# Optimization experiments

Hardware: AMD Instinct MI355X
Metric: run time of the kernel (lower is better)

Reference implementation:

```python
import jax, jax.numpy as jnp
import numpy as np

SIZE = 512
ATTN = 64      # per-head attention_size
OUT = 64       # per-head output_size
HEADS = 8

def setup_inputs() -> dict:
    key = jax.random.key(0)
    ks = jax.random.split(key, 7)
    s = 0.02
    return {
        "x":  jax.random.normal(ks[0], (4, 2048, SIZE), dtype=jnp.float32),
        "Wq": jax.random.normal(ks[1], (SIZE, ATTN * HEADS), dtype=jnp.float32) * s,
        "bq": jax.random.normal(ks[2], (ATTN * HEADS,), dtype=jnp.float32) * s,
        "Wk": jax.random.normal(ks[3], (SIZE, ATTN), dtype=jnp.float32) * s,  # shared key, no bias
        "Wv": jax.random.normal(ks[4], (SIZE, OUT * HEADS), dtype=jnp.float32) * s,
        "bv": jax.random.normal(ks[5], (OUT * HEADS,), dtype=jnp.float32) * s,
    }

def reference(x, Wq, bq, Wk, Wv, bv):
    B, S, _ = x.shape
    q = (x @ Wq + bq).reshape(B, S, HEADS, ATTN)   # (B,S,H,A)
    k = x @ Wk                                      # (B,S,A) shared across heads
    v = (x @ Wv + bv).reshape(B, S, HEADS, OUT)     # (B,S,H,O)
    # NOTE: original divides by sqrt(seq_len), not sqrt(head_dim)
    scale = 1.0 / np.sqrt(S).astype(np.float32)
    scores = jnp.einsum("bqha,bka->bhqk", q, k) * scale  # (B,H,S,S)
    causal = jnp.tril(jnp.ones((S, S), dtype=bool))
    scores = jnp.where(causal, scores, -jnp.inf)
    attn = jax.nn.softmax(scores, axis=-1)
    out = jnp.einsum("bhqk,bkho->bqho", attn, v)    # (B,S,H,O)
    return out.reshape(B, S, HEADS * OUT)
```

## Files before the change

kernel.cpp:

```cpp
#include <hip/hip_runtime.h>
#include <math.h>


typedef _Float16 half8 __attribute__((ext_vector_type(8)));
typedef _Float16 half4 __attribute__((ext_vector_type(4)));
typedef float float4v __attribute__((ext_vector_type(4)));
typedef unsigned int u32;

#define SCL2E 0.031885926f

__device__ inline float4v mfma16(half8 a, half8 b, float4v c) {
    return __builtin_amdgcn_mfma_f32_16x16x32_f16(a, b, c, 0, 0, 0);
}
__device__ inline void load16(const _Float16* g, _Float16* l) {
    __builtin_amdgcn_global_load_lds((const __attribute__((address_space(1))) u32*)g,
                                     (__attribute__((address_space(3))) u32*)l, 16, 0, 0);
}

__global__ __launch_bounds__(256) void prep(
    const float* __restrict__ x, const float* __restrict__ Wq,
    const float* __restrict__ Wk, const float* __restrict__ Wv,
    _Float16* __restrict__ xh, _Float16* __restrict__ wqt,
    _Float16* __restrict__ wkt, _Float16* __restrict__ wvt) {
    const int bid = blockIdx.x;
    if (bid < 2048) {
        size_t base = (size_t)bid * 2048 + (size_t)threadIdx.x * 8;
        const float4* xp = (const float4*)(x + base);
        float4 f0 = xp[0], f1 = xp[1];
        half8 h = {(_Float16)f0.x, (_Float16)f0.y, (_Float16)f0.z, (_Float16)f0.w,
                   (_Float16)f1.x, (_Float16)f1.y, (_Float16)f1.z, (_Float16)f1.w};
        *(half8*)(xh + base) = h;
    } else {
        int r = bid - 2048;
        const float* W; _Float16* WT; int N, bx, by;
        if (r < 256)      { W = Wq; WT = wqt; N = 512; bx = r & 15; by = r >> 4; }
        else if (r < 288) { r -= 256; W = Wk; WT = wkt; N = 64;  bx = r & 1;  by = r >> 1; }
        else              { r -= 288; W = Wv; WT = wvt; N = 512; bx = r & 15; by = r >> 4; }
        __shared__ float T[32][33];
        const int tx = threadIdx.x & 31, ty = threadIdx.x >> 5;
        const int n0 = bx * 32, k0 = by * 32;
#pragma unroll
        for (int i = 0; i < 4; ++i)
            T[ty + 8 * i][tx] = W[(size_t)(k0 + ty + 8 * i) * N + n0 + tx];
        __syncthreads();
#pragma unroll
        for (int i = 0; i < 4; ++i)
            WT[(size_t)(n0 + ty + 8 * i) * 512 + k0 + tx] = (_Float16)T[tx][ty + 8 * i];
    }
}

__global__ __launch_bounds__(256) void qkv_gemm(
    const _Float16* __restrict__ xh,
    const _Float16* __restrict__ wqt, const _Float16* __restrict__ wkt,
    const _Float16* __restrict__ wvt,
    const float* __restrict__ bq, const float* __restrict__ bv,
    _Float16* __restrict__ q_ws, _Float16* __restrict__ kt_ws, _Float16* __restrict__ vt_ws) {
    __shared__ __align__(16) _Float16 Xs[2][8192];
    __shared__ __align__(16) _Float16 Ws[2][4096];

    const int m0 = blockIdx.x * 128;
    const int nt = blockIdx.y;
    const _Float16* WT;
    const float* bias;
    if (nt < 8)       { WT = wqt + (size_t)nt * 64 * 512; bias = bq + nt * 64; }
    else if (nt == 8) { WT = wkt;                          bias = nullptr; }
    else              { WT = wvt + (size_t)(nt - 9) * 64 * 512; bias = bv + (nt - 9) * 64; }

    const int tid = threadIdx.x;
    const int w = tid >> 6, lane = tid & 63, quad = lane >> 4, cl = lane & 15;
    const int lrow = lane >> 3;
    const int lgc = (lane & 7) ^ lrow;
    const _Float16* xg = xh + (size_t)(m0 + lrow) * 512 + lgc * 8;
    const _Float16* wg = WT + (size_t)lrow * 512 + lgc * 8;

    const int g0 = (quad ^ (cl & 7)) << 3;
    const int g1 = ((quad ^ 4) ^ (cl & 7)) << 3;

    float4v acc[2][4] = {};

#pragma unroll
    for (int c = 0; c < 4; ++c) {
        int cc = w * 4 + c;
        load16(xg + (size_t)cc * 8 * 512, Xs[0] + cc * 512);
    }
#pragma unroll
    for (int c = 0; c < 2; ++c) {
        int cc = w * 2 + c;
        load16(wg + (size_t)cc * 8 * 512, Ws[0] + cc * 512);
    }

    for (int ki = 0; ki < 8; ++ki) {
        const int cb = ki & 1, nb = cb ^ 1;
        __syncthreads();
        if (ki < 7) {
            const int kk = (ki + 1) * 64;
#pragma unroll
            for (int c = 0; c < 4; ++c) {
                int cc = w * 4 + c;
                load16(xg + (size_t)cc * 8 * 512 + kk, Xs[nb] + cc * 512);
            }
#pragma unroll
            for (int c = 0; c < 2; ++c) {
                int cc = w * 2 + c;
                load16(wg + (size_t)cc * 8 * 512 + kk, Ws[nb] + cc * 512);
            }
        }
#pragma unroll
        for (int c = 0; c < 2; ++c) {
            const int g = c ? g1 : g0;
#pragma unroll
            for (int s = 0; s < 2; ++s) {
                half8 a = *(const half8*)(Xs[cb] + (w * 32 + s * 16 + cl) * 64 + g);
#pragma unroll
                for (int j = 0; j < 4; ++j) {
                    half8 b = *(const half8*)(Ws[cb] + (j * 16 + cl) * 64 + g);
                    acc[s][j] = mfma16(a, b, acc[s][j]);
                }
            }
        }
    }

    if (nt < 8) {
#pragma unroll
        for (int s = 0; s < 2; ++s)
#pragma unroll
            for (int j = 0; j < 4; ++j)
#pragma unroll
                for (int r = 0; r < 4; ++r) {
                    int lr = w * 32 + s * 16 + quad * 4 + r;
                    int col = j * 16 + cl;
                    q_ws[(size_t)(m0 + lr) * 512 + nt * 64 + col] =
                        (_Float16)((acc[s][j][r] + bias[col]) * SCL2E);
                }
    } else if (nt == 8) {
#pragma unroll
        for (int s = 0; s < 2; ++s)
#pragma unroll
            for (int j = 0; j < 4; ++j)
#pragma unroll
                for (int r = 0; r < 4; ++r) {
                    int grow = m0 + w * 32 + s * 16 + quad * 4 + r;
                    int b = grow >> 11, t = (grow >> 6) & 31, row = grow & 63;
                    int col = j * 16 + cl;
                    kt_ws[((size_t)(b * 32 + t) << 12) + row * 64 +
                          (((col >> 3) ^ (row & 7)) << 3) + (col & 7)] = (_Float16)acc[s][j][r];
                }
    } else {
        const int h = nt - 9;
#pragma unroll
        for (int s = 0; s < 2; ++s)
#pragma unroll
            for (int j = 0; j < 4; ++j)
#pragma unroll
                for (int r = 0; r < 4; ++r) {
                    int grow = m0 + w * 32 + s * 16 + quad * 4 + r;
                    int b = grow >> 11, t = (grow >> 6) & 31, row = grow & 63;
                    int o = j * 16 + cl;
                    int kap = ((row & 15) << 2) + (row >> 4);
                    vt_ws[(((size_t)(b * 8 + h) * 32 + t) << 12) + o * 64 +
                          (((kap >> 3) ^ (o & 7)) << 3) + (kap & 7)] =
                        (_Float16)(acc[s][j][r] + bias[o]);
                }
    }
}

__global__ __launch_bounds__(512, 2) void attn(
    const _Float16* __restrict__ q_ws, const _Float16* __restrict__ kt_ws,
    const _Float16* __restrict__ vt_ws, float* __restrict__ out) {
    __shared__ __align__(16) _Float16 Ks[2][2][4096];
    __shared__ __align__(16) _Float16 VTs[2][2][4096];
    __shared__ __align__(16) _Float16 Ps[8][1024];

    const int bh = blockIdx.x, b = bh >> 3, h = bh & 7;
    const int p = 31 - blockIdx.y;
    const int q0 = p * 64;
    const int nmax = (p + 2) >> 1;

    const int bS = b * 2048;
    const int tid = threadIdx.x;
    const int w = tid >> 6, lane = tid & 63, quad = lane >> 4, cl = lane & 15;
    const int g = w >> 2, wl = w & 3;
    const int tbase = g ? nmax : 0;
    const int nit = g ? (p + 1 - nmax) : nmax;

    const _Float16* kbase = kt_ws + ((size_t)(b * 32) << 12);
    const _Float16* vbase = vt_ws + ((size_t)((b * 8 + h) * 32) << 12);

    const int g0 = (quad ^ (cl & 7)) << 3;
    const int g1 = ((quad ^ 4) ^ (cl & 7)) << 3;
    const int so0 = wl * 1024 + lane * 8;

    const _Float16* qbase = q_ws + (size_t)(bS + q0 + wl * 16 + cl) * 512 + h * 64;
    half8 qa0 = *(const half8*)(qbase + quad * 8);
    half8 qa1 = *(const half8*)(qbase + 32 + quad * 8);

    float4v oacc[4] = {};
    float l_run[4] = {0.f, 0.f, 0.f, 0.f};

    _Float16* KsG = &Ks[g][0][0];
    _Float16* VsG = &VTs[g][0][0];

    auto stageK = [&](int tile, int buf) {
        const _Float16* kt = kbase + ((size_t)tile << 12);
        load16(kt + so0,       KsG + buf * 4096 + wl * 1024);
        load16(kt + so0 + 512, KsG + buf * 4096 + wl * 1024 + 512);
    };
    auto stageV = [&](int tile, int buf) {
        const _Float16* vt = vbase + ((size_t)tile << 12);
        load16(vt + so0,       VsG + buf * 4096 + wl * 1024);
        load16(vt + so0 + 512, VsG + buf * 4096 + wl * 1024 + 512);
    };
    auto qk_sm = [&](int tg, int buf) {
        const _Float16* KB = KsG + buf * 4096;
        if (tg != p) {
            float4v sfr[4];
#pragma unroll
            for (int j = 0; j < 4; ++j) {
                const _Float16* kr = KB + (j * 16 + cl) * 64;
                half8 b0 = *(const half8*)(kr + g0);
                half8 b1 = *(const half8*)(kr + g1);
                float4v a_ = {0.f, 0.f, 0.f, 0.f};
                a_ = mfma16(qa0, b0, a_);
                a_ = mfma16(qa1, b1, a_);
                sfr[j] = a_;
            }
#pragma unroll
            for (int r = 0; r < 4; ++r) {
                float p0 = exp2f(sfr[0][r]), p1 = exp2f(sfr[1][r]);
                float p2 = exp2f(sfr[2][r]), p3 = exp2f(sfr[3][r]);
                l_run[r] += (p0 + p1) + (p2 + p3);
                int rr = quad * 4 + r;
                half4 ph = {(_Float16)p0, (_Float16)p1, (_Float16)p2, (_Float16)p3};
                *(half4*)&Ps[w][rr * 64 + ((((cl >> 1) ^ (rr & 7)) << 3) | ((cl & 1) << 2))] = ph;
            }
        } else {
            const int jmax = wl;
            float4v sfr[4];
#pragma unroll
            for (int j = 0; j < 4; ++j) {
                if (j <= jmax) {
                    const _Float16* kr = KB + (j * 16 + cl) * 64;
                    half8 b0 = *(const half8*)(kr + g0);
                    half8 b1 = *(const half8*)(kr + g1);
                    float4v a_ = {0.f, 0.f, 0.f, 0.f};
                    a_ = mfma16(qa0, b0, a_);
                    a_ = mfma16(qa1, b1, a_);
                    sfr[j] = a_;
                }
            }
#pragma unroll
            for (int r = 0; r < 4; ++r) {
                float pj[4];
#pragma unroll
                for (int j = 0; j < 4; ++j) {
                    bool live = (j < jmax) || (j == jmax && cl <= quad * 4 + r);
                    pj[j] = live ? exp2f(sfr[j][r]) : 0.f;
                }
                l_run[r] += (pj[0] + pj[1]) + (pj[2] + pj[3]);
                int rr = quad * 4 + r;
                half4 ph = {(_Float16)pj[0], (_Float16)pj[1], (_Float16)pj[2], (_Float16)pj[3]};
                *(half4*)&Ps[w][rr * 64 + ((((cl >> 1) ^ (rr & 7)) << 3) | ((cl & 1) << 2))] = ph;
            }
        }
    };
    auto pv = [&](int buf) {
        const _Float16* PB = &Ps[w][cl * 64];
        half8 pa0 = *(const half8*)(PB + g0);
        half8 pa1 = *(const half8*)(PB + g1);
        const _Float16* VB = VsG + buf * 4096;
#pragma unroll
        for (int jo = 0; jo < 4; ++jo) {
            const _Float16* vr = VB + (jo * 16 + cl) * 64;
            half8 v0 = *(const half8*)(vr + g0);
            half8 v1 = *(const half8*)(vr + g1);
            oacc[jo] = mfma16(pa0, v0, oacc[jo]);
            oacc[jo] = mfma16(pa1, v1, oacc[jo]);
        }
    };

    if (nit > 0) {
        stageK(tbase, 0);
        if (g == 0) stageV(tbase, 0);
    }

    for (int t = 0; t < nmax; ++t) {
        const int cb = t & 1, nb = cb ^ 1;
        __syncthreads();
        const int tg = tbase + t;
        if (g == 0) {
            if (t + 1 < nit) { stageK(tg + 1, nb); stageV(tg + 1, nb); }
            qk_sm(tg, cb);
            pv(cb);
        } else {
            if (t > 0 && t - 1 < nit) pv(nb);
            if (t + 1 < nit) stageK(tg + 1, nb);
            if (t < nit) {
                stageV(tg, cb);
                qk_sm(tg, cb);
            }
        }
    }

    __syncthreads();
    if (g == 1 && nit == nmax) pv((nmax - 1) & 1);

    float* Obuf = (float*)&Ks[1][0][0];
    float* Lbuf = (float*)&VTs[0][0][0];
    if (g == 1) {
#pragma unroll
        for (int jo = 0; jo < 4; ++jo)
#pragma unroll
            for (int r = 0; r < 4; ++r) {
                int row = wl * 16 + quad * 4 + r;
                Obuf[row * 64 + jo * 16 + cl] = oacc[jo][r];
            }
#pragma unroll
        for (int r = 0; r < 4; ++r) {
            int row = wl * 16 + quad * 4 + r;
            Lbuf[row * 16 + cl] = l_run[r];
        }
    }
    __syncthreads();
    if (g == 0) {
#pragma unroll
        for (int r = 0; r < 4; ++r) {
            int row = wl * 16 + quad * 4 + r;
            float l = l_run[r] + Lbuf[row * 16 + cl];
            l += __shfl_xor(l, 1);
            l += __shfl_xor(l, 2);
            l += __shfl_xor(l, 4);
            l += __shfl_xor(l, 8);
            float inv = 1.0f / l;
            float* op = out + (size_t)(bS + q0 + row) * 512 + h * 64 + cl;
            op[0]  = (oacc[0][r] + Obuf[row * 64 +      cl]) * inv;
            op[16] = (oacc[1][r] + Obuf[row * 64 + 16 + cl]) * inv;
            op[32] = (oacc[2][r] + Obuf[row * 64 + 32 + cl]) * inv;
            op[48] = (oacc[3][r] + Obuf[row * 64 + 48 + cl]) * inv;
        }
    }
}

extern "C" void kernel_launch(void* const* d_in, const int* in_sizes, int n_in,
                              void* d_out, int out_size, void* d_ws, size_t ws_size,
                              hipStream_t stream) {
    const float* x  = (const float*)d_in[0];
    const float* Wq = (const float*)d_in[1];
    const float* bq = (const float*)d_in[2];
    const float* Wk = (const float*)d_in[3];
    const float* Wv = (const float*)d_in[4];
    const float* bv = (const float*)d_in[5];
    float* out = (float*)d_out;

    char* ws = (char*)d_ws;
    _Float16* q_ws  = (_Float16*)(ws);
    _Float16* kt_ws = (_Float16*)(ws + 8388608);
    _Float16* vt_ws = (_Float16*)(ws + 9437184);
    _Float16* wqt   = (_Float16*)(ws + 17825792);
    _Float16* wkt   = (_Float16*)(ws + 18350080);
    _Float16* wvt   = (_Float16*)(ws + 18415616);
    _Float16* xh    = (_Float16*)(ws + 18939904);

    prep<<<dim3(2592), dim3(256), 0, stream>>>(x, Wq, Wk, Wv, xh, wqt, wkt, wvt);

    qkv_gemm<<<dim3(64, 17), dim3(256), 0, stream>>>(
        xh, wqt, wkt, wvt, bq, bv, q_ws, kt_ws, vt_ws);

    attn<<<dim3(32, 32), dim3(512), 0, stream>>>(q_ws, kt_ws, vt_ws, out);
}
```

Baseline: 137.9 us.

## Widen QKV GEMM tiles to 128x128 with 512 threads and add MFMA priority hints

The QKV projection GEMM now computes 128 output columns per block with 8 waves (one 16-row strip each) instead of 64 columns with 4 waves. This halves the grid's y dimension and the number of times each X tile is reloaded from global memory. The shared-key tile stays 64 wide and guards its loads. s_setprio hints are also placed around the MFMA sections in both the GEMM and the attention kernel so matrix work gets issue priority over other waves. In exchange there are fewer blocks in the grid, more LDS per block, and per-wave register pressure changes.

```diff
diff --git a/kernel.cpp b/kernel.cpp
--- a/kernel.cpp
+++ b/kernel.cpp
@@ -49,22 +49,22 @@
     }
 }
 
-__global__ __launch_bounds__(256) void qkv_gemm(
+__global__ __launch_bounds__(512) void qkv_gemm(
     const _Float16* __restrict__ xh,
     const _Float16* __restrict__ wqt, const _Float16* __restrict__ wkt,
     const _Float16* __restrict__ wvt,
     const float* __restrict__ bq, const float* __restrict__ bv,
     _Float16* __restrict__ q_ws, _Float16* __restrict__ kt_ws, _Float16* __restrict__ vt_ws) {
     __shared__ __align__(16) _Float16 Xs[2][8192];
-    __shared__ __align__(16) _Float16 Ws[2][4096];
+    __shared__ __align__(16) _Float16 Ws[2][8192];
 
     const int m0 = blockIdx.x * 128;
-    const int nt = blockIdx.y;
+    const int y = blockIdx.y;
     const _Float16* WT;
-    const float* bias;
-    if (nt < 8)       { WT = wqt + (size_t)nt * 64 * 512; bias = bq + nt * 64; }
-    else if (nt == 8) { WT = wkt;                          bias = nullptr; }
-    else              { WT = wvt + (size_t)(nt - 9) * 64 * 512; bias = bv + (nt - 9) * 64; }
+    if (y < 4)       { WT = wqt + (size_t)y * 128 * 512; }
+    else if (y == 4) { WT = wkt; }
+    else             { WT = wvt + (size_t)(y - 5) * 128 * 512; }
+    const int wcn = (y == 4) ? 8 : 16;
 
     const int tid = threadIdx.x;
     const int w = tid >> 6, lane = tid & 63, quad = lane >> 4, cl = lane & 15;
@@ -76,91 +76,90 @@
     const int g0 = (quad ^ (cl & 7)) << 3;
     const int g1 = ((quad ^ 4) ^ (cl & 7)) << 3;
 
-    float4v acc[2][4] = {};
-
-#pragma unroll
-    for (int c = 0; c < 4; ++c) {
-        int cc = w * 4 + c;
-        load16(xg + (size_t)cc * 8 * 512, Xs[0] + cc * 512);
-    }
-#pragma unroll
-    for (int c = 0; c < 2; ++c) {
-        int cc = w * 2 + c;
-        load16(wg + (size_t)cc * 8 * 512, Ws[0] + cc * 512);
-    }
+    float4v acc[8] = {};
+
+    auto stage = [&](int kk, int buf) {
+#pragma unroll
+        for (int c = 0; c < 2; ++c) {
+            int cc = w * 2 + c;
+            load16(xg + (size_t)cc * 8 * 512 + kk, Xs[buf] + cc * 512);
+        }
+#pragma unroll
+        for (int c = 0; c < 2; ++c) {
+            int cc = w * 2 + c;
+            if (cc < wcn)
+                load16(wg + (size_t)cc * 8 * 512 + kk, Ws[buf] + cc * 512);
+        }
+    };
+
+    stage(0, 0);
 
     for (int ki = 0; ki < 8; ++ki) {
         const int cb = ki & 1, nb = cb ^ 1;
         __syncthreads();
-        if (ki < 7) {
-            const int kk = (ki + 1) * 64;
-#pragma unroll
-            for (int c = 0; c < 4; ++c) {
-                int cc = w * 4 + c;
-                load16(xg + (size_t)cc * 8 * 512 + kk, Xs[nb] + cc * 512);
-            }
+        if (ki < 7) stage((ki + 1) * 64, nb);
+        __builtin_amdgcn_s_setprio(1);
+        if (y != 4) {
 #pragma unroll
             for (int c = 0; c < 2; ++c) {
-                int cc = w * 2 + c;
-                load16(wg + (size_t)cc * 8 * 512 + kk, Ws[nb] + cc * 512);
-            }
-        }
-#pragma unroll
-        for (int c = 0; c < 2; ++c) {
-            const int g = c ? g1 : g0;
-#pragma unroll
-            for (int s = 0; s < 2; ++s) {
-                half8 a = *(const half8*)(Xs[cb] + (w * 32 + s * 16 + cl) * 64 + g);
+                const int g = c ? g1 : g0;
+                half8 a = *(const half8*)(Xs[cb] + (w * 16 + cl) * 64 + g);
+#pragma unroll
+                for (int j = 0; j < 8; ++j) {
+                    half8 b = *(const half8*)(Ws[cb] + (j * 16 + cl) * 64 + g);
+                    acc[j] = mfma16(a, b, acc[j]);
+                }
+            }
+        } else {
+#pragma unroll
+            for (int c = 0; c < 2; ++c) {
+                const int g = c ? g1 : g0;
+                half8 a = *(const half8*)(Xs[cb] + (w * 16 + cl) * 64 + g);
 #pragma unroll
                 for (int j = 0; j < 4; ++j) {
                     half8 b = *(const half8*)(Ws[cb] + (j * 16 + cl) * 64 + g);
-                    acc[s][j] = mfma16(a, b, acc[s][j]);
+                    acc[j] = mfma16(a, b, acc[j]);
                 }
             }
         }
-    }
-
-    if (nt < 8) {
-#pragma unroll
-        for (int s = 0; s < 2; ++s)
-#pragma unroll
-            for (int j = 0; j < 4; ++j)
-#pragma unroll
-                for (int r = 0; r < 4; ++r) {
-                    int lr = w * 32 + s * 16 + quad * 4 + r;
-                    int col = j * 16 + cl;
-                    q_ws[(size_t)(m0 + lr) * 512 + nt * 64 + col] =
-                        (_Float16)((acc[s][j][r] + bias[col]) * SCL2E);
-                }
-    } else if (nt == 8) {
-#pragma unroll
-        for (int s = 0; s < 2; ++s)
-#pragma unroll
-            for (int j = 0; j < 4; ++j)
-#pragma unroll
-                for (int r = 0; r < 4; ++r) {
-                    int grow = m0 + w * 32 + s * 16 + quad * 4 + r;
-                    int b = grow >> 11, t = (grow >> 6) & 31, row = grow & 63;
-                    int col = j * 16 + cl;
-                    kt_ws[((size_t)(b * 32 + t) << 12) + row * 64 +
-                          (((col >> 3) ^ (row & 7)) << 3) + (col & 7)] = (_Float16)acc[s][j][r];
-                }
+        __builtin_amdgcn_s_setprio(0);
+    }
+
+    if (y < 4) {
+#pragma unroll
+        for (int j = 0; j < 8; ++j)
+#pragma unroll
+            for (int r = 0; r < 4; ++r) {
+                int lr = w * 16 + quad * 4 + r;
+                int col = y * 128 + j * 16 + cl;
+                q_ws[(size_t)(m0 + lr) * 512 + col] =
+                    (_Float16)((acc[j][r] + bq[col]) * SCL2E);
+            }
+    } else if (y == 4) {
+#pragma unroll
+        for (int j = 0; j < 4; ++j)
+#pragma unroll
+            for (int r = 0; r < 4; ++r) {
+                int grow = m0 + w * 16 + quad * 4 + r;
+                int b = grow >> 11, t = (grow >> 6) & 31, row = grow & 63;
+                int col = j * 16 + cl;
+                kt_ws[((size_t)(b * 32 + t) << 12) + row * 64 +
+                      (((col >> 3) ^ (row & 7)) << 3) + (col & 7)] = (_Float16)acc[j][r];
+            }
     } else {
-        const int h = nt - 9;
-#pragma unroll
-        for (int s = 0; s < 2; ++s)
-#pragma unroll
-            for (int j = 0; j < 4; ++j)
-#pragma unroll
-                for (int r = 0; r < 4; ++r) {
-                    int grow = m0 + w * 32 + s * 16 + quad * 4 + r;
-                    int b = grow >> 11, t = (grow >> 6) & 31, row = grow & 63;
-                    int o = j * 16 + cl;
-                    int kap = ((row & 15) << 2) + (row >> 4);
-                    vt_ws[(((size_t)(b * 8 + h) * 32 + t) << 12) + o * 64 +
-                          (((kap >> 3) ^ (o & 7)) << 3) + (kap & 7)] =
-                        (_Float16)(acc[s][j][r] + bias[o]);
-                }
+#pragma unroll
+        for (int j = 0; j < 8; ++j)
+#pragma unroll
+            for (int r = 0; r < 4; ++r) {
+                int grow = m0 + w * 16 + quad * 4 + r;
+                int b = grow >> 11, t = (grow >> 6) & 31, row = grow & 63;
+                int h = (y - 5) * 2 + (j >> 2);
+                int o = (j & 3) * 16 + cl;
+                int kap = ((row & 15) << 2) + (row >> 4);
+                vt_ws[(((size_t)(b * 8 + h) * 32 + t) << 12) + o * 64 +
+                      (((kap >> 3) ^ (o & 7)) << 3) + (kap & 7)] =
+                    (_Float16)(acc[j][r] + bv[h * 64 + o]);
+            }
     }
 }
 
@@ -214,6 +213,7 @@
         const _Float16* KB = KsG + buf * 4096;
         if (tg != p) {
             float4v sfr[4];
+            __builtin_amdgcn_s_setprio(1);
 #pragma unroll
             for (int j = 0; j < 4; ++j) {
                 const _Float16* kr = KB + (j * 16 + cl) * 64;
@@ -224,6 +224,7 @@
                 a_ = mfma16(qa1, b1, a_);
                 sfr[j] = a_;
             }
+            __builtin_amdgcn_s_setprio(0);
 #pragma unroll
             for (int r = 0; r < 4; ++r) {
                 float p0 = exp2f(sfr[0][r]), p1 = exp2f(sfr[1][r]);
@@ -268,6 +269,7 @@
         half8 pa0 = *(const half8*)(PB + g0);
         half8 pa1 = *(const half8*)(PB + g1);
         const _Float16* VB = VsG + buf * 4096;
+        __builtin_amdgcn_s_setprio(1);
 #pragma unroll
         for (int jo = 0; jo < 4; ++jo) {
             const _Float16* vr = VB + (jo * 16 + cl) * 64;
@@ -276,6 +278,7 @@
             oacc[jo] = mfma16(pa0, v0, oacc[jo]);
             oacc[jo] = mfma16(pa1, v1, oacc[jo]);
         }
+        __builtin_amdgcn_s_setprio(0);
     };
 
     if (nit > 0) {
@@ -362,7 +365,7 @@
 
     prep<<<dim3(2592), dim3(256), 0, stream>>>(x, Wq, Wk, Wv, xh, wqt, wkt, wvt);
 
-    qkv_gemm<<<dim3(64, 17), dim3(256), 0, stream>>>(
+    qkv_gemm<<<dim3(64, 9), dim3(512), 0, stream>>>(
         xh, wqt, wkt, wvt, bq, bv, q_ws, kt_ws, vt_ws);
 
     attn<<<dim3(32, 32), dim3(512), 0, stream>>>(q_ws, kt_ws, vt_ws, out);
```

New measurement: 145.5 us. +5.5%, slower.

## Widen QKV GEMM tiles to 128 columns and drop LDS double buffering

Applied to the files above, without the earlier changes.

The QKV projection GEMM now computes 128 output columns per block (two heads) instead of 64, which cuts the grid from 17 to 9 column tiles and halves how often each X tile is re-read. The shared K projection keeps a 64-wide special path. LDS double buffering is replaced by single buffers with a sync before and after each load, so global loads no longer overlap with MFMA work. Each block holds twice as many accumulators, which may raise register pressure, and the grid now has fewer blocks.

```diff
diff --git a/kernel.cpp b/kernel.cpp
--- a/kernel.cpp
+++ b/kernel.cpp
@@ -55,16 +55,15 @@
     const _Float16* __restrict__ wvt,
     const float* __restrict__ bq, const float* __restrict__ bv,
     _Float16* __restrict__ q_ws, _Float16* __restrict__ kt_ws, _Float16* __restrict__ vt_ws) {
-    __shared__ __align__(16) _Float16 Xs[2][8192];
-    __shared__ __align__(16) _Float16 Ws[2][4096];
+    __shared__ __align__(16) _Float16 Xs[8192];
+    __shared__ __align__(16) _Float16 Ws[8192];
 
     const int m0 = blockIdx.x * 128;
-    const int nt = blockIdx.y;
+    const int y = blockIdx.y;
     const _Float16* WT;
-    const float* bias;
-    if (nt < 8)       { WT = wqt + (size_t)nt * 64 * 512; bias = bq + nt * 64; }
-    else if (nt == 8) { WT = wkt;                          bias = nullptr; }
-    else              { WT = wvt + (size_t)(nt - 9) * 64 * 512; bias = bv + (nt - 9) * 64; }
+    if (y < 4)       { WT = wqt + (size_t)y * 128 * 512; }
+    else if (y == 4) { WT = wkt; }
+    else             { WT = wvt + (size_t)(y - 5) * 128 * 512; }
 
     const int tid = threadIdx.x;
     const int w = tid >> 6, lane = tid & 63, quad = lane >> 4, cl = lane & 15;
@@ -76,63 +75,74 @@
     const int g0 = (quad ^ (cl & 7)) << 3;
     const int g1 = ((quad ^ 4) ^ (cl & 7)) << 3;
 
-    float4v acc[2][4] = {};
-
-#pragma unroll
-    for (int c = 0; c < 4; ++c) {
-        int cc = w * 4 + c;
-        load16(xg + (size_t)cc * 8 * 512, Xs[0] + cc * 512);
-    }
-#pragma unroll
-    for (int c = 0; c < 2; ++c) {
-        int cc = w * 2 + c;
-        load16(wg + (size_t)cc * 8 * 512, Ws[0] + cc * 512);
-    }
+    float4v acc[2][8] = {};
 
     for (int ki = 0; ki < 8; ++ki) {
-        const int cb = ki & 1, nb = cb ^ 1;
+        const int kk = ki * 64;
         __syncthreads();
-        if (ki < 7) {
-            const int kk = (ki + 1) * 64;
+#pragma unroll
+        for (int c = 0; c < 4; ++c) {
+            int cc = w * 4 + c;
+            load16(xg + (size_t)cc * 8 * 512 + kk, Xs + cc * 512);
+        }
+        if (y != 4) {
 #pragma unroll
             for (int c = 0; c < 4; ++c) {
                 int cc = w * 4 + c;
-                load16(xg + (size_t)cc * 8 * 512 + kk, Xs[nb] + cc * 512);
-            }
+                load16(wg + (size_t)cc * 8 * 512 + kk, Ws + cc * 512);
+            }
+        } else {
 #pragma unroll
             for (int c = 0; c < 2; ++c) {
                 int cc = w * 2 + c;
-                load16(wg + (size_t)cc * 8 * 512 + kk, Ws[nb] + cc * 512);
-            }
-        }
-#pragma unroll
-        for (int c = 0; c < 2; ++c) {
-            const int g = c ? g1 : g0;
-#pragma unroll
-            for (int s = 0; s < 2; ++s) {
-                half8 a = *(const half8*)(Xs[cb] + (w * 32 + s * 16 + cl) * 64 + g);
-#pragma unroll
-                for (int j = 0; j < 4; ++j) {
-                    half8 b = *(const half8*)(Ws[cb] + (j * 16 + cl) * 64 + g);
-                    acc[s][j] = mfma16(a, b, acc[s][j]);
-                }
-            }
-        }
-    }
-
-    if (nt < 8) {
+                load16(wg + (size_t)cc * 8 * 512 + kk, Ws + cc * 512);
+            }
+        }
+        __syncthreads();
+        if (y != 4) {
+#pragma unroll
+            for (int c = 0; c < 2; ++c) {
+                const int g = c ? g1 : g0;
+#pragma unroll
+                for (int s = 0; s < 2; ++s) {
+                    half8 a = *(const half8*)(Xs + (w * 32 + s * 16 + cl) * 64 + g);
+#pragma unroll
+                    for (int j = 0; j < 8; ++j) {
+                        half8 b = *(const half8*)(Ws + (j * 16 + cl) * 64 + g);
+                        acc[s][j] = mfma16(a, b, acc[s][j]);
+                    }
+                }
+            }
+        } else {
+#pragma unroll
+            for (int c = 0; c < 2; ++c) {
+                const int g = c ? g1 : g0;
+#pragma unroll
+                for (int s = 0; s < 2; ++s) {
+                    half8 a = *(const half8*)(Xs + (w * 32 + s * 16 + cl) * 64 + g);
+#pragma unroll
+                    for (int j = 0; j < 4; ++j) {
+                        half8 b = *(const half8*)(Ws + (j * 16 + cl) * 64 + g);
+                        acc[s][j] = mfma16(a, b, acc[s][j]);
+                    }
+                }
+            }
+        }
+    }
+
+    if (y < 4) {
 #pragma unroll
         for (int s = 0; s < 2; ++s)
 #pragma unroll
-            for (int j = 0; j < 4; ++j)
+            for (int j = 0; j < 8; ++j)
 #pragma unroll
                 for (int r = 0; r < 4; ++r) {
                     int lr = w * 32 + s * 16 + quad * 4 + r;
-                    int col = j * 16 + cl;
-                    q_ws[(size_t)(m0 + lr) * 512 + nt * 64 + col] =
-                        (_Float16)((acc[s][j][r] + bias[col]) * SCL2E);
-                }
-    } else if (nt == 8) {
+                    int col = y * 128 + j * 16 + cl;
+                    q_ws[(size_t)(m0 + lr) * 512 + col] =
+                        (_Float16)((acc[s][j][r] + bq[col]) * SCL2E);
+                }
+    } else if (y == 4) {
 #pragma unroll
         for (int s = 0; s < 2; ++s)
 #pragma unroll
@@ -146,20 +156,20 @@
                           (((col >> 3) ^ (row & 7)) << 3) + (col & 7)] = (_Float16)acc[s][j][r];
                 }
     } else {
-        const int h = nt - 9;
 #pragma unroll
         for (int s = 0; s < 2; ++s)
 #pragma unroll
-            for (int j = 0; j < 4; ++j)
+            for (int j = 0; j < 8; ++j)
 #pragma unroll
                 for (int r = 0; r < 4; ++r) {
                     int grow = m0 + w * 32 + s * 16 + quad * 4 + r;
                     int b = grow >> 11, t = (grow >> 6) & 31, row = grow & 63;
-                    int o = j * 16 + cl;
+                    int h = (y - 5) * 2 + (j >> 2);
+                    int o = (j & 3) * 16 + cl;
                     int kap = ((row & 15) << 2) + (row >> 4);
                     vt_ws[(((size_t)(b * 8 + h) * 32 + t) << 12) + o * 64 +
                           (((kap >> 3) ^ (o & 7)) << 3) + (kap & 7)] =
-                        (_Float16)(acc[s][j][r] + bias[o]);
+                        (_Float16)(acc[s][j][r] + bv[h * 64 + o]);
                 }
     }
 }
@@ -362,7 +372,7 @@
 
     prep<<<dim3(2592), dim3(256), 0, stream>>>(x, Wq, Wk, Wv, xh, wqt, wkt, wvt);
 
-    qkv_gemm<<<dim3(64, 17), dim3(256), 0, stream>>>(
+    qkv_gemm<<<dim3(64, 9), dim3(256), 0, stream>>>(
         xh, wqt, wkt, wvt, bq, bv, q_ws, kt_ws, vt_ws);
 
     attn<<<dim3(32, 32), dim3(512), 0, stream>>>(q_ws, kt_ws, vt_ws, out);
```

New measurement: 147.1 us. 1.07x slower.

## Give each attention wave two 16-row query tiles, halving block size

Applied to the files above, without the earlier changes.

The attention kernel drops from 8 waves to 4 per block, and each wave now handles 32 query rows as two 16-row subtiles. Each K/V fragment read from LDS then feeds twice as many MFMAs, which cuts LDS traffic per FLOP, and staging loads per thread double. The cost is more registers per wave (two sets of accumulators and scores) and fewer waves per block to hide latency, which could hurt occupancy.

```diff
diff --git a/kernel.cpp b/kernel.cpp
--- a/kernel.cpp
+++ b/kernel.cpp
@@ -164,12 +164,12 @@
     }
 }
 
-__global__ __launch_bounds__(512, 2) void attn(
+__global__ __launch_bounds__(256, 2) void attn(
     const _Float16* __restrict__ q_ws, const _Float16* __restrict__ kt_ws,
     const _Float16* __restrict__ vt_ws, float* __restrict__ out) {
     __shared__ __align__(16) _Float16 Ks[2][2][4096];
     __shared__ __align__(16) _Float16 VTs[2][2][4096];
-    __shared__ __align__(16) _Float16 Ps[8][1024];
+    __shared__ __align__(16) _Float16 Ps[4][2048];
 
     const int bh = blockIdx.x, b = bh >> 3, h = bh & 7;
     const int p = 31 - blockIdx.y;
@@ -179,7 +179,7 @@
     const int bS = b * 2048;
     const int tid = threadIdx.x;
     const int w = tid >> 6, lane = tid & 63, quad = lane >> 4, cl = lane & 15;
-    const int g = w >> 2, wl = w & 3;
+    const int g = w >> 1, wl = w & 1;
     const int tbase = g ? nmax : 0;
     const int nit = g ? (p + 1 - nmax) : nmax;
 
@@ -188,93 +188,118 @@
 
     const int g0 = (quad ^ (cl & 7)) << 3;
     const int g1 = ((quad ^ 4) ^ (cl & 7)) << 3;
-    const int so0 = wl * 1024 + lane * 8;
-
-    const _Float16* qbase = q_ws + (size_t)(bS + q0 + wl * 16 + cl) * 512 + h * 64;
-    half8 qa0 = *(const half8*)(qbase + quad * 8);
-    half8 qa1 = *(const half8*)(qbase + 32 + quad * 8);
-
-    float4v oacc[4] = {};
-    float l_run[4] = {0.f, 0.f, 0.f, 0.f};
+    const int so0 = wl * 2048 + lane * 8;
+    const int sd0 = wl * 2048;
+
+    half8 qa[2][2];
+#pragma unroll
+    for (int s = 0; s < 2; ++s) {
+        const _Float16* qb = q_ws + (size_t)(bS + q0 + wl * 32 + s * 16 + cl) * 512 + h * 64;
+        qa[s][0] = *(const half8*)(qb + quad * 8);
+        qa[s][1] = *(const half8*)(qb + 32 + quad * 8);
+    }
+
+    float4v oacc[2][4] = {};
+    float l_run[2][4] = {};
 
     _Float16* KsG = &Ks[g][0][0];
     _Float16* VsG = &VTs[g][0][0];
 
     auto stageK = [&](int tile, int buf) {
         const _Float16* kt = kbase + ((size_t)tile << 12);
-        load16(kt + so0,       KsG + buf * 4096 + wl * 1024);
-        load16(kt + so0 + 512, KsG + buf * 4096 + wl * 1024 + 512);
+#pragma unroll
+        for (int c = 0; c < 4; ++c)
+            load16(kt + so0 + c * 512, KsG + buf * 4096 + sd0 + c * 512);
     };
     auto stageV = [&](int tile, int buf) {
         const _Float16* vt = vbase + ((size_t)tile << 12);
-        load16(vt + so0,       VsG + buf * 4096 + wl * 1024);
-        load16(vt + so0 + 512, VsG + buf * 4096 + wl * 1024 + 512);
+#pragma unroll
+        for (int c = 0; c < 4; ++c)
+            load16(vt + so0 + c * 512, VsG + buf * 4096 + sd0 + c * 512);
     };
     auto qk_sm = [&](int tg, int buf) {
         const _Float16* KB = KsG + buf * 4096;
         if (tg != p) {
-            float4v sfr[4];
+            float4v sfr[2][4];
 #pragma unroll
             for (int j = 0; j < 4; ++j) {
                 const _Float16* kr = KB + (j * 16 + cl) * 64;
                 half8 b0 = *(const half8*)(kr + g0);
                 half8 b1 = *(const half8*)(kr + g1);
-                float4v a_ = {0.f, 0.f, 0.f, 0.f};
-                a_ = mfma16(qa0, b0, a_);
-                a_ = mfma16(qa1, b1, a_);
-                sfr[j] = a_;
-            }
-#pragma unroll
-            for (int r = 0; r < 4; ++r) {
-                float p0 = exp2f(sfr[0][r]), p1 = exp2f(sfr[1][r]);
-                float p2 = exp2f(sfr[2][r]), p3 = exp2f(sfr[3][r]);
-                l_run[r] += (p0 + p1) + (p2 + p3);
-                int rr = quad * 4 + r;
-                half4 ph = {(_Float16)p0, (_Float16)p1, (_Float16)p2, (_Float16)p3};
-                *(half4*)&Ps[w][rr * 64 + ((((cl >> 1) ^ (rr & 7)) << 3) | ((cl & 1) << 2))] = ph;
-            }
+#pragma unroll
+                for (int s = 0; s < 2; ++s) {
+                    float4v a_ = {0.f, 0.f, 0.f, 0.f};
+                    a_ = mfma16(qa[s][0], b0, a_);
+                    a_ = mfma16(qa[s][1], b1, a_);
+                    sfr[s][j] = a_;
+                }
+            }
+#pragma unroll
+            for (int s = 0; s < 2; ++s)
+#pragma unroll
+                for (int r = 0; r < 4; ++r) {
+                    float p0 = exp2f(sfr[s][0][r]), p1 = exp2f(sfr[s][1][r]);
+                    float p2 = exp2f(sfr[s][2][r]), p3 = exp2f(sfr[s][3][r]);
+                    l_run[s][r] += (p0 + p1) + (p2 + p3);
+                    int rr = s * 16 + quad * 4 + r;
+                    half4 ph = {(_Float16)p0, (_Float16)p1, (_Float16)p2, (_Float16)p3};
+                    *(half4*)&Ps[w][rr * 64 + ((((cl >> 1) ^ (rr & 7)) << 3) | ((cl & 1) << 2))] = ph;
+                }
         } else {
-            const int jmax = wl;
-            float4v sfr[4];
+            float4v sfr[2][4];
 #pragma unroll
             for (int j = 0; j < 4; ++j) {
-                if (j <= jmax) {
+                if (j <= wl * 2 + 1) {
                     const _Float16* kr = KB + (j * 16 + cl) * 64;
                     half8 b0 = *(const half8*)(kr + g0);
                     half8 b1 = *(const half8*)(kr + g1);
-                    float4v a_ = {0.f, 0.f, 0.f, 0.f};
-                    a_ = mfma16(qa0, b0, a_);
-                    a_ = mfma16(qa1, b1, a_);
-                    sfr[j] = a_;
-                }
-            }
-#pragma unroll
-            for (int r = 0; r < 4; ++r) {
-                float pj[4];
-#pragma unroll
-                for (int j = 0; j < 4; ++j) {
-                    bool live = (j < jmax) || (j == jmax && cl <= quad * 4 + r);
-                    pj[j] = live ? exp2f(sfr[j][r]) : 0.f;
-                }
-                l_run[r] += (pj[0] + pj[1]) + (pj[2] + pj[3]);
-                int rr = quad * 4 + r;
-                half4 ph = {(_Float16)pj[0], (_Float16)pj[1], (_Float16)pj[2], (_Float16)pj[3]};
-                *(half4*)&Ps[w][rr * 64 + ((((cl >> 1) ^ (rr & 7)) << 3) | ((cl & 1) << 2))] = ph;
+#pragma unroll
+                    for (int s = 0; s < 2; ++s) {
+                        if (j <= wl * 2 + s) {
+                            float4v a_ = {0.f, 0.f, 0.f, 0.f};
+                            a_ = mfma16(qa[s][0], b0, a_);
+                            a_ = mfma16(qa[s][1], b1, a_);
+                            sfr[s][j] = a_;
+                        }
+                    }
+                }
+            }
+#pragma unroll
+            for (int s = 0; s < 2; ++s) {
+                const int jmax = wl * 2 + s;
+#pragma unroll
+                for (int r = 0; r < 4; ++r) {
+                    float pj[4];
+#pragma unroll
+                    for (int j = 0; j < 4; ++j) {
+                        bool live = (j < jmax) || (j == jmax && cl <= quad * 4 + r);
+                        pj[j] = live ? exp2f(sfr[s][j][r]) : 0.f;
+                    }
+                    l_run[s][r] += (pj[0] + pj[1]) + (pj[2] + pj[3]);
+                    int rr = s * 16 + quad * 4 + r;
+                    half4 ph = {(_Float16)pj[0], (_Float16)pj[1], (_Float16)pj[2], (_Float16)pj[3]};
+                    *(half4*)&Ps[w][rr * 64 + ((((cl >> 1) ^ (rr & 7)) << 3) | ((cl & 1) << 2))] = ph;
+                }
             }
         }
     };
     auto pv = [&](int buf) {
-        const _Float16* PB = &Ps[w][cl * 64];
-        half8 pa0 = *(const half8*)(PB + g0);
-        half8 pa1 = *(const half8*)(PB + g1);
+        const _Float16* PB0 = &Ps[w][cl * 64];
+        const _Float16* PB1 = &Ps[w][(16 + cl) * 64];
+        half8 pa00 = *(const half8*)(PB0 + g0);
+        half8 pa01 = *(const half8*)(PB0 + g1);
+        half8 pa10 = *(const half8*)(PB1 + g0);
+        half8 pa11 = *(const half8*)(PB1 + g1);
         const _Float16* VB = VsG + buf * 4096;
 #pragma unroll
         for (int jo = 0; jo < 4; ++jo) {
             const _Float16* vr = VB + (jo * 16 + cl) * 64;
             half8 v0 = *(const half8*)(vr + g0);
             half8 v1 = *(const half8*)(vr + g1);
-            oacc[jo] = mfma16(pa0, v0, oacc[jo]);
-            oacc[jo] = mfma16(pa1, v1, oacc[jo]);
+            oacc[0][jo] = mfma16(pa00, v0, oacc[0][jo]);
+            oacc[0][jo] = mfma16(pa01, v1, oacc[0][jo]);
+            oacc[1][jo] = mfma16(pa10, v0, oacc[1][jo]);
+            oacc[1][jo] = mfma16(pa11, v1, oacc[1][jo]);
         }
     };
 
@@ -308,35 +333,41 @@
     float* Lbuf = (float*)&VTs[0][0][0];
     if (g == 1) {
 #pragma unroll
-        for (int jo = 0; jo < 4; ++jo)
+        for (int s = 0; s < 2; ++s)
+#pragma unroll
+            for (int jo = 0; jo < 4; ++jo)
+#pragma unroll
+                for (int r = 0; r < 4; ++r) {
+                    int row = wl * 32 + s * 16 + quad * 4 + r;
+                    Obuf[row * 64 + jo * 16 + cl] = oacc[s][jo][r];
+                }
+#pragma unroll
+        for (int s = 0; s < 2; ++s)
 #pragma unroll
             for (int r = 0; r < 4; ++r) {
-                int row = wl * 16 + quad * 4 + r;
-                Obuf[row * 64 + jo * 16 + cl] = oacc[jo][r];
-            }
-#pragma unroll
-        for (int r = 0; r < 4; ++r) {
-            int row = wl * 16 + quad * 4 + r;
-            Lbuf[row * 16 + cl] = l_run[r];
-        }
+                int row = wl * 32 + s * 16 + quad * 4 + r;
+                Lbuf[row * 16 + cl] = l_run[s][r];
+            }
     }
     __syncthreads();
     if (g == 0) {
 #pragma unroll
-        for (int r = 0; r < 4; ++r) {
-            int row = wl * 16 + quad * 4 + r;
-            float l = l_run[r] + Lbuf[row * 16 + cl];
-            l += __shfl_xor(l, 1);
-            l += __shfl_xor(l, 2);
-            l += __shfl_xor(l, 4);
-            l += __shfl_xor(l, 8);
-            float inv = 1.0f / l;
-            float* op = out + (size_t)(bS + q0 + row) * 512 + h * 64 + cl;
-            op[0]  = (oacc[0][r] + Obuf[row * 64 +      cl]) * inv;
-            op[16] = (oacc[1][r] + Obuf[row * 64 + 16 + cl]) * inv;
-            op[32] = (oacc[2][r] + Obuf[row * 64 + 32 + cl]) * inv;
-            op[48] = (oacc[3][r] + Obuf[row * 64 + 48 + cl]) * inv;
-        }
+        for (int s = 0; s < 2; ++s)
+#pragma unroll
+            for (int r = 0; r < 4; ++r) {
+                int row = wl * 32 + s * 16 + quad * 4 + r;
+                float l = l_run[s][r] + Lbuf[row * 16 + cl];
+                l += __shfl_xor(l, 1);
+                l += __shfl_xor(l, 2);
+                l += __shfl_xor(l, 4);
+                l += __shfl_xor(l, 8);
+                float inv = 1.0f / l;
+                float* op = out + (size_t)(bS + q0 + row) * 512 + h * 64 + cl;
+                op[0]  = (oacc[s][0][r] + Obuf[row * 64 +      cl]) * inv;
+                op[16] = (oacc[s][1][r] + Obuf[row * 64 + 16 + cl]) * inv;
+                op[32] = (oacc[s][2][r] + Obuf[row * 64 + 32 + cl]) * inv;
+                op[48] = (oacc[s][3][r] + Obuf[row * 64 + 48 + cl]) * inv;
+            }
     }
 }
 
@@ -365,5 +396,5 @@
     qkv_gemm<<<dim3(64, 17), dim3(256), 0, stream>>>(
         xh, wqt, wkt, wvt, bq, bv, q_ws, kt_ws, vt_ws);
 
-    attn<<<dim3(32, 32), dim3(512), 0, stream>>>(q_ws, kt_ws, vt_ws, out);
-}
+    attn<<<dim3(32, 32), dim3(256), 0, stream>>>(q_ws, kt_ws, vt_ws, out);
+}
```

Result: slower. 142.8 us (+3.6%).
